# Optimization experiments

Measured on AMD Instinct MI355X. Metric: run time of the kernel, lower is better.

The kernel has to match this reference:

```python
import jax, jax.numpy as jnp
import numpy as np
from jax import lax

WS = 7            # window size
DIM = 256         # out_dim
HEADS = 8
HD = DIM // HEADS # head dim = 32
HIDDEN = 4 * DIM  # mlp hidden = 1024
IN_DIM = 512
EPS = 1e-6

def _rel_pos_index(ws):
    coords = np.stack(np.meshgrid(np.arange(ws), np.arange(ws), indexing='ij'))
    cf = coords.reshape(2, -1)
    rc = (cf[:, :, None] - cf[:, None, :]).transpose(1, 2, 0)
    rc[:, :, 0] += ws - 1
    rc[:, :, 1] += ws - 1
    rc[:, :, 0] *= 2 * ws - 1
    return rc.sum(-1)  # (N, N)

RPI = jnp.asarray(_rel_pos_index(WS))  # (49, 49) int

def _layernorm(x, g, b):
    m = jnp.mean(x, axis=-1, keepdims=True)
    v = jnp.mean(jnp.square(x - m), axis=-1, keepdims=True)
    return (x - m) * lax.rsqrt(v + EPS) * g + b

def setup_inputs() -> dict:
    key = jax.random.key(0)
    ks = jax.random.split(key, 16)
    s = 0.02
    inp = {
        'x': jax.random.normal(ks[0], (8, IN_DIM, 48, 48), jnp.float32),
        'skip_feat': jax.random.normal(ks[1], (8, DIM, 96, 96), jnp.float32),
        # ConvTranspose2d(in, out, k=2, s=2): weight (in, out, 2, 2), bias (out,)
        'up_w': jax.random.normal(ks[2], (IN_DIM, DIM, 2, 2), jnp.float32) * s,
        'up_b': jnp.zeros((DIM,), jnp.float32),
        # skip_adapter Conv2d(out, out, 1, bias=False)
        'skip_w': jax.random.normal(ks[3], (DIM, DIM, 1, 1), jnp.float32) * s,
        'gamma1': jnp.ones((DIM,), jnp.float32),
        'beta1': jnp.zeros((DIM,), jnp.float32),
        'qkv_w': jax.random.normal(ks[4], (3 * DIM, DIM), jnp.float32) * s,
        'qkv_b': jnp.zeros((3 * DIM,), jnp.float32),
        'rpb_table': jax.random.normal(ks[5], ((2 * WS - 1) ** 2, HEADS), jnp.float32) * s,
        'proj_w': jax.random.normal(ks[6], (DIM, DIM), jnp.float32) * s,
        'proj_b': jnp.zeros((DIM,), jnp.float32),
        'gamma2': jnp.ones((DIM,), jnp.float32),
        'beta2': jnp.zeros((DIM,), jnp.float32),
        'mlp_w1': jax.random.normal(ks[7], (HIDDEN, DIM), jnp.float32) * s,
        'mlp_b1': jnp.zeros((HIDDEN,), jnp.float32),
        'mlp_w2': jax.random.normal(ks[8], (DIM, HIDDEN), jnp.float32) * s,
        'mlp_b2': jnp.zeros((DIM,), jnp.float32),
    }
    return inp

def _forward(x, skip_feat, up_w, up_b, skip_w, gamma1, beta1, qkv_w, qkv_b,
             rpb_table, proj_w, proj_b, gamma2, beta2, mlp_w1, mlp_b1, mlp_w2, mlp_b2):
    B = x.shape[0]
    # ConvTranspose2d k=2 s=2 p=0 == lhs-dilated conv with spatially flipped kernel
    y = lax.conv_general_dilated(
        x, jnp.flip(up_w, (2, 3)), window_strides=(1, 1),
        padding=((1, 1), (1, 1)), lhs_dilation=(2, 2),
        dimension_numbers=('NCHW', 'IOHW', 'NCHW')) + up_b[None, :, None, None]
    shortcut = y  # (B, C, Hup, Wup)
    # skip adapter (1x1 conv, no bias); shapes match so no interpolate/adhoc conv
    y = y + jnp.einsum('oi,bihw->bohw', skip_w[:, :, 0, 0], skip_feat)
    xh = jnp.transpose(y, (0, 2, 3, 1))  # (B, H, W, C)
    H, W, C = xh.shape[1], xh.shape[2], xh.shape[3]
    xn = _layernorm(xh, gamma1, beta1)
    pad_b = (WS - H % WS) % WS
    pad_r = (WS - W % WS) % WS
    xp = jnp.pad(xn, ((0, 0), (0, pad_b), (0, pad_r), (0, 0)))
    Hp, Wp = H + pad_b, W + pad_r
    N = WS * WS
    # window partition -> (B * nWh * nWw, N, C)
    win = xp.reshape(B, Hp // WS, WS, Wp // WS, WS, C)
    win = jnp.transpose(win, (0, 1, 3, 2, 4, 5)).reshape(-1, N, C)
    B_ = win.shape[0]
    # attention
    qkv = (win @ qkv_w.T + qkv_b).reshape(B_, N, 3, HEADS, HD)
    qkv = jnp.transpose(qkv, (2, 0, 3, 1, 4))  # (3, B_, h, N, hd)
    q, k, v = qkv[0], qkv[1], qkv[2]
    attn = jnp.einsum('bhnd,bhmd->bhnm', q * (HD ** -0.5), k)
    bias = rpb_table[RPI.reshape(-1)].reshape(N, N, HEADS)
    attn = attn + jnp.transpose(bias, (2, 0, 1))[None]  # (B_, h, N, N)
    attn = jax.nn.softmax(attn, axis=-1)
    o = jnp.einsum('bhnm,bhmd->bhnd', attn, v)
    o = jnp.transpose(o, (0, 2, 1, 3)).reshape(B_, N, C)
    o = o @ proj_w.T + proj_b
    # window reverse + crop
    o = o.reshape(B, Hp // WS, Wp // WS, WS, WS, C)
    o = jnp.transpose(o, (0, 1, 3, 2, 4, 5)).reshape(B, Hp, Wp, C)[:, :H, :W]
    x2 = jnp.transpose(shortcut, (0, 2, 3, 1)) + o
    # MLP
    h = jax.nn.gelu(_layernorm(x2, gamma2, beta2) @ mlp_w1.T + mlp_b1, approximate=False)
    x3 = x2 + (h @ mlp_w2.T + mlp_b2)
    return jnp.transpose(x3, (0, 3, 1, 2))  # (B, C, Hup, Wup)

def reference(x, skip_feat, up_w, up_b, skip_w, gamma1, beta1, qkv_w, qkv_b,
              rpb_table, proj_w, proj_b, gamma2, beta2, mlp_w1, mlp_b1, mlp_w2, mlp_b2):
    return _forward(x, skip_feat, up_w, up_b, skip_w, gamma1, beta1, qkv_w, qkv_b,
                    rpb_table, proj_w, proj_b, gamma2, beta2, mlp_w1, mlp_b1, mlp_w2, mlp_b2)
```

## Files before the change

### kernel.cpp

```cpp
#include <hip/hip_runtime.h>

typedef __attribute__((ext_vector_type(8))) short short8;
typedef __attribute__((ext_vector_type(4))) float f32x4;
typedef __attribute__((ext_vector_type(4))) unsigned short u16x4;
typedef unsigned short u16;
typedef unsigned int u32;

#define DEV static __device__ __forceinline__

DEV u16 f2b(float f) {
  u32 u = __builtin_bit_cast(u32, f);
  return (u16)((u + 0x7fffu + ((u >> 16) & 1u)) >> 16);
}
DEV float b2f(u16 h) {
  u32 u = ((u32)h) << 16;
  return __builtin_bit_cast(float, u);
}
DEV short8 ld8(const u16* p) { return *reinterpret_cast<const short8*>(p); }
DEV f32x4 mfma16(short8 a, short8 b, f32x4 c) {
  return __builtin_amdgcn_mfma_f32_16x16x32_bf16(a, b, c, 0, 0, 0);
}
DEV float wredsum(float v) {
#pragma unroll
  for (int off = 1; off < 64; off <<= 1) v += __shfl_xor(v, off);
  return v;
}

#define GLL(gp, lp) __builtin_amdgcn_global_load_lds( \
    (const __attribute__((address_space(1))) void*)(gp), \
    (__attribute__((address_space(3))) void*)(lp), 16, 0, 0)

#define WQKV   0
#define WPROJ  196608
#define WM1    262144
#define WM2    524288
#define WSKIP  786432
#define WUP    851968

#define OFF_BIAS 2752512u
#define OFF_SC   2883584u
#define OFF_OVR  40632320u
#define OFF_STAT (OFF_OVR + 52000000u)
#define OFF_PST  (OFF_OVR + 52600000u)
#define OFF_SGB  (OFF_OVR + 55000000u)
#define WS_NEED  96227328u

__global__ void k_sentinel(float* out) { out[threadIdx.x] = 31337.0f; }

__global__ __launch_bounds__(256) void k_prep(
    const float* qkv_w, const float* proj_w, const float* mlp_w1,
    const float* mlp_w2, const float* skip_w, const float* up_w,
    const float* rpb, const float* g1, const float* g2, u16* W, float* bias_g) {
  int i = blockIdx.x * 256 + threadIdx.x;
  if (i < 196608) { W[WQKV + i] = f2b(qkv_w[i] * g1[i & 255]); return; }
  i -= 196608;
  if (i < 65536) { W[WPROJ + i] = f2b(proj_w[i]); return; }
  i -= 65536;
  if (i < 262144) { W[WM1 + i] = f2b(mlp_w1[i] * g2[i & 255]); return; }
  i -= 262144;
  if (i < 262144) { W[WM2 + i] = f2b(mlp_w2[i]); return; }
  i -= 262144;
  if (i < 65536) { W[WSKIP + i] = f2b(skip_w[i]); return; }
  i -= 65536;
  if (i < 524288) {
    int ci = i & 511; int rest = i >> 9; int co = rest & 255; int kk = rest >> 8;
    W[WUP + i] = f2b(up_w[ci * 1024 + co * 4 + kk]);
    return;
  }
  i -= 524288;
  if (i < 32768) {
    int h = i >> 12, r = i & 4095, ii = r >> 6, j = r & 63;
    float v;
    if (j >= 49) v = -1e30f;
    else if (ii >= 49) v = 0.f;
    else {
      int d0 = (ii / 7 - j / 7) + 6, d1 = (ii % 7 - j % 7) + 6;
      v = rpb[(d0 * 13 + d1) * 8 + h];
    }
    bias_g[i] = v;
  }
}

__global__ __launch_bounds__(256) void k_fold(
    const float* mlp_w1, const float* qkv_w, const float* g1, const float* be1,
    const float* g2, const float* be2, float* sgb) {
  int wave = threadIdx.x >> 6, lane = threadIdx.x & 63;
  int id = blockIdx.x * 4 + wave;
  const float* wsrc;
  const float* vec;
  int out;
  if (id < 1024) { wsrc = mlp_w1 + (size_t)id * 256; vec = g2; out = id; }
  else if (id < 2048) { wsrc = mlp_w1 + (size_t)(id - 1024) * 256; vec = be2; out = id; }
  else { wsrc = qkv_w + (size_t)(id - 2048) * 256; vec = be1; out = 2816 + (id - 2048); }
  float s = 0.f;
#pragma unroll
  for (int j = 0; j < 4; j++) {
    int k = j * 64 + lane;
    s += vec[k] * wsrc[k];
  }
  s = wredsum(s);
  if (lane == 0) sgb[out] = s;
}

__global__ __launch_bounds__(256) void k_tr(const float* src, u16* dst, int C, int HW) {
  __shared__ float t[32][33];
  int hw0 = blockIdx.x * 32, c0 = blockIdx.y * 32, b = blockIdx.z;
  int tx = threadIdx.x & 31, ty = threadIdx.x >> 5;
  const float* s = src + (size_t)b * C * HW;
  u16* d = dst + (size_t)b * C * HW;
#pragma unroll
  for (int i = 0; i < 4; i++)
    t[ty + i * 8][tx] = s[(size_t)(c0 + ty + i * 8) * HW + hw0 + tx];
  __syncthreads();
#pragma unroll
  for (int i = 0; i < 4; i++)
    d[(size_t)(hw0 + ty + i * 8) * C + c0 + tx] = f2b(t[tx][ty + i * 8]);
}

__global__ __launch_bounds__(256) void k_tr_skip(const float* src, u16* dst) {
  __shared__ float t[32][33];
  int w0 = blockIdx.x * 32, c0 = blockIdx.y * 32;
  int z = blockIdx.z;
  int b = z / 96, h = z - b * 96;
  int tx = threadIdx.x & 31, ty = threadIdx.x >> 5;
  const float* s = src + (size_t)b * 256 * 9216 + (size_t)h * 96;
  u16* d = dst + (((size_t)b * 96 + h) * 96) * 256;
#pragma unroll
  for (int i = 0; i < 4; i++)
    t[ty + i * 8][tx] = s[(size_t)(c0 + ty + i * 8) * 9216 + w0 + tx];
  __syncthreads();
#pragma unroll
  for (int i = 0; i < 4; i++)
    d[(size_t)(w0 + ty + i * 8) * 256 + c0 + tx] = f2b(t[tx][ty + i * 8]);
}

__global__ __launch_bounds__(256) void k1g(
    const u16* W, const u16* xt, const float* up_b, u16* sc) {
  __shared__ __align__(16) u16 Ab[2][4096];
  __shared__ __align__(16) u16 Bb[2][4096];
  int tid = threadIdx.x;
  int lane = tid & 63, wave = tid >> 6;
  int m = lane & 15, gq = lane >> 4;
  int wr = wave >> 1, wc = wave & 1;
  int bm = blockIdx.x * 128, bn = blockIdx.y * 128;
  int kk = blockIdx.z, kh = kk >> 1, kw = kk & 1;
  const u16* Ag = xt + (size_t)bm * 512;
  const u16* Bg = W + WUP + (size_t)kk * 131072 + (size_t)bn * 512;
  f32x4 acc[4][4] = {};
#pragma unroll
  for (int c = 0; c < 2; c++) {
    int flat = (wave * 2 + c) * 512 + lane * 8;
    int r = flat >> 5, cc = flat & 31;
    GLL(Ag + (size_t)r * 512 + cc, &Ab[0][(wave * 2 + c) * 512]);
    GLL(Bg + (size_t)r * 512 + cc, &Bb[0][(wave * 2 + c) * 512]);
  }
  __syncthreads();
  int cur = 0;
  for (int ki = 0; ki < 16; ki++) {
    if (ki < 15) {
      int kkk = (ki + 1) * 32;
#pragma unroll
      for (int c = 0; c < 2; c++) {
        int flat = (wave * 2 + c) * 512 + lane * 8;
        int r = flat >> 5, cc = flat & 31;
        GLL(Ag + (size_t)r * 512 + kkk + cc, &Ab[cur ^ 1][(wave * 2 + c) * 512]);
        GLL(Bg + (size_t)r * 512 + kkk + cc, &Bb[cur ^ 1][(wave * 2 + c) * 512]);
      }
    }
    short8 aF[4], bF[4];
#pragma unroll
    for (int mt = 0; mt < 4; mt++)
      aF[mt] = ld8(&Ab[cur][(wr * 64 + mt * 16 + m) * 32 + gq * 8]);
#pragma unroll
    for (int nt = 0; nt < 4; nt++)
      bF[nt] = ld8(&Bb[cur][(wc * 64 + nt * 16 + m) * 32 + gq * 8]);
#pragma unroll
    for (int mt = 0; mt < 4; mt++)
#pragma unroll
      for (int nt = 0; nt < 4; nt++)
        acc[mt][nt] = mfma16(aF[mt], bF[nt], acc[mt][nt]);
    __syncthreads();
    cur ^= 1;
  }
  float ub[4];
#pragma unroll
  for (int nt = 0; nt < 4; nt++) ub[nt] = up_b[bn + wc * 64 + nt * 16 + m];
#pragma unroll
  for (int mt = 0; mt < 4; mt++)
#pragma unroll
    for (int rr = 0; rr < 4; rr++) {
      int t = bm + wr * 64 + mt * 16 + gq * 4 + rr;
      int b = t / 2304, rem = t - b * 2304;
      int ih = rem / 48, iw = rem - ih * 48;
      int h = 2 * ih + kh, w = 2 * iw + kw;
      size_t tok = ((size_t)b * 96 + h) * 96 + w;
#pragma unroll
      for (int nt = 0; nt < 4; nt++) {
        int ch = bn + wc * 64 + nt * 16 + m;
        sc[tok * 256 + ch] = f2b(acc[mt][nt][rr] + ub[nt]);
      }
    }
}

__global__ __launch_bounds__(256) void k2y(
    const u16* W, const u16* skt, const u16* sc, u16* ybuf, float* pstat) {
  __shared__ __align__(16) u16 Ab[2][4096];
  __shared__ __align__(16) u16 Bb[2][4096];
  int tid = threadIdx.x;
  int lane = tid & 63, wave = tid >> 6;
  int m = lane & 15, gq = lane >> 4;
  int wr = wave >> 1, wc = wave & 1;
  int bm = blockIdx.x * 128, bn = blockIdx.y * 128;
  const u16* Ag = skt + (size_t)bm * 256;
  const u16* Bg = W + WSKIP + (size_t)bn * 256;
  f32x4 acc[4][4] = {};
#pragma unroll
  for (int c = 0; c < 2; c++) {
    int flat = (wave * 2 + c) * 512 + lane * 8;
    int r = flat >> 5, cc = flat & 31;
    GLL(Ag + (size_t)r * 256 + cc, &Ab[0][(wave * 2 + c) * 512]);
    GLL(Bg + (size_t)r * 256 + cc, &Bb[0][(wave * 2 + c) * 512]);
  }
  __syncthreads();
  int cur = 0;
  for (int ki = 0; ki < 8; ki++) {
    if (ki < 7) {
      int kk = (ki + 1) * 32;
#pragma unroll
      for (int c = 0; c < 2; c++) {
        int flat = (wave * 2 + c) * 512 + lane * 8;
        int r = flat >> 5, cc = flat & 31;
        GLL(Ag + (size_t)r * 256 + kk + cc, &Ab[cur ^ 1][(wave * 2 + c) * 512]);
        GLL(Bg + (size_t)r * 256 + kk + cc, &Bb[cur ^ 1][(wave * 2 + c) * 512]);
      }
    }
    short8 aF[4], bF[4];
#pragma unroll
    for (int mt = 0; mt < 4; mt++)
      aF[mt] = ld8(&Ab[cur][(wr * 64 + mt * 16 + m) * 32 + gq * 8]);
#pragma unroll
    for (int nt = 0; nt < 4; nt++)
      bF[nt] = ld8(&Bb[cur][(wc * 64 + nt * 16 + m) * 32 + gq * 8]);
#pragma unroll
    for (int mt = 0; mt < 4; mt++)
#pragma unroll
      for (int nt = 0; nt < 4; nt++)
        acc[mt][nt] = mfma16(aF[mt], bF[nt], acc[mt][nt]);
    __syncthreads();
    cur ^= 1;
  }
#pragma unroll
  for (int mt = 0; mt < 4; mt++)
#pragma unroll
    for (int rr = 0; rr < 4; rr++) {
      int tok = bm + wr * 64 + mt * 16 + gq * 4 + rr;
      float s = 0.f, s2 = 0.f;
#pragma unroll
      for (int nt = 0; nt < 4; nt++) {
        int ch = bn + wc * 64 + nt * 16 + m;
        float y = acc[mt][nt][rr] + b2f(sc[(size_t)tok * 256 + ch]);
        ybuf[(size_t)tok * 256 + ch] = f2b(y);
        s += y; s2 += y * y;
      }
#pragma unroll
      for (int off = 1; off < 16; off <<= 1) {
        s += __shfl_xor(s, off);
        s2 += __shfl_xor(s2, off);
      }
      if (m == 0) {
        int pi = (tok * 4 + blockIdx.y * 2 + wc) * 2;
        pstat[pi] = s;
        pstat[pi + 1] = s2;
      }
    }
}

__global__ __launch_bounds__(256) void k_statfin(const float* pstat, float* stat) {
  int row = blockIdx.x * 256 + threadIdx.x;
  float s = 0.f, s2 = 0.f;
#pragma unroll
  for (int j = 0; j < 4; j++) {
    s += pstat[(row * 4 + j) * 2];
    s2 += pstat[(row * 4 + j) * 2 + 1];
  }
  float mean = s * 0.00390625f;
  float var = s2 * 0.00390625f - mean * mean;
  float r = rsqrtf(var + 1e-6f);
  stat[row * 2] = r;
  stat[row * 2 + 1] = r * mean;
}

__global__ __launch_bounds__(256) void k23(
    const u16* W, const u16* ybuf, const float* stat, const float* sgb,
    const float* qkv_b, const float* bias_g, u16* obr) {
  __shared__ __align__(16) u16 yl[49 * 264];
  __shared__ __align__(16) u16 pws[4][6144];
  int tid = threadIdx.x;
  int lane = tid & 63, wave = tid >> 6;
  int m = lane & 15, gq = lane >> 4, k0 = gq * 8;
  int blk = blockIdx.x;
  int bimg = blk / 196, wl = blk - bimg * 196;
  int wrow = wl / 14, wcol = wl - wrow * 14;
  int h0 = wrow * 7, w0 = wcol * 7;
  u16* prv = pws[wave];
#pragma unroll
  for (int t = 0; t < 8; t++) {
    u16x4 z = {};
    *reinterpret_cast<u16x4*>(&prv[t * 256 + lane * 4]) = z;
  }
  for (int it = 0; it < 7; it++) {
    int flat = it * 256 + tid;
    if (flat < 1568) {
      int row = flat >> 5, cc = (flat & 31) * 8;
      int hh = h0 + row / 7, ww = w0 + row % 7;
      short8 v = {};
      if (hh < 96 && ww < 96) {
        int ras = (bimg * 96 + hh) * 96 + ww;
        short8 raw = ld8(ybuf + (size_t)ras * 256 + cc);
        float rs = stat[ras * 2], rmu = stat[ras * 2 + 1];
#pragma unroll
        for (int q2 = 0; q2 < 8; q2++) {
          float zz = b2f(((const u16*)&raw)[q2]) * rs - rmu;
          ((u16*)&v)[q2] = f2b(zz);
        }
      }
      *reinterpret_cast<short8*>(&yl[row * 264 + cc]) = v;
    }
  }
  __syncthreads();
  const float scale = 0.1767766952966369f;
#pragma unroll
  for (int hp = 0; hp < 2; hp++) {
    int h = wave * 2 + hp;
    {
      const u16* bb0 = W + WQKV + (size_t)(h * 32 + m) * 256;
      const u16* bb1 = W + WQKV + (size_t)(h * 32 + 16 + m) * 256;
      const u16* bb2 = W + WQKV + (size_t)(256 + h * 32 + m) * 256;
      const u16* bb3 = W + WQKV + (size_t)(256 + h * 32 + 16 + m) * 256;
      f32x4 acc[4][4] = {};
#pragma unroll 4
      for (int ks = 0; ks < 8; ks++) {
        short8 a[4];
#pragma unroll
        for (int mt = 0; mt < 4; mt++) {
          int row = mt * 16 + m; if (row > 48) row = 48;
          a[mt] = ld8(&yl[row * 264 + ks * 32 + k0]);
        }
        short8 b0 = ld8(bb0 + ks * 32 + k0);
        short8 b1 = ld8(bb1 + ks * 32 + k0);
        short8 b2 = ld8(bb2 + ks * 32 + k0);
        short8 b3 = ld8(bb3 + ks * 32 + k0);
#pragma unroll
        for (int mt = 0; mt < 4; mt++) {
          acc[mt][0] = mfma16(a[mt], b0, acc[mt][0]);
          acc[mt][1] = mfma16(a[mt], b1, acc[mt][1]);
          acc[mt][2] = mfma16(a[mt], b2, acc[mt][2]);
          acc[mt][3] = mfma16(a[mt], b3, acc[mt][3]);
        }
      }
#pragma unroll
      for (int nt = 0; nt < 4; nt++) {
        int hd = (nt & 1) * 16 + m;
        int c = (nt >> 1) * 256 + h * 32 + hd;
        float qb_ = qkv_b[c];
        float sb1 = sgb[2816 + c];
        int base = (nt < 2) ? 2048 : 3616;
#pragma unroll
        for (int mt = 0; mt < 4; mt++)
#pragma unroll
          for (int rr = 0; rr < 4; rr++) {
            int row = mt * 16 + gq * 4 + rr;
            if (row >= 49) continue;
            int hh = h0 + row / 7, ww = w0 + row % 7;
            float vf = (hh < 96 && ww < 96) ? 1.f : 0.f;
            prv[base + row * 32 + hd] = f2b(acc[mt][nt][rr] + vf * sb1 + qb_);
          }
      }
    }
    {
      const u16* bb0 = W + WQKV + (size_t)(512 + h * 32 + m) * 256;
      const u16* bb1 = W + WQKV + (size_t)(512 + h * 32 + 16 + m) * 256;
      f32x4 vacc[4][2] = {};
#pragma unroll 4
      for (int ks = 0; ks < 8; ks++) {
        short8 a[4];
#pragma unroll
        for (int mt = 0; mt < 4; mt++) {
          int row = mt * 16 + m; if (row > 48) row = 48;
          a[mt] = ld8(&yl[row * 264 + ks * 32 + k0]);
        }
        short8 b0 = ld8(bb0 + ks * 32 + k0);
        short8 b1 = ld8(bb1 + ks * 32 + k0);
#pragma unroll
        for (int mt = 0; mt < 4; mt++) {
          vacc[mt][0] = mfma16(a[mt], b0, vacc[mt][0]);
          vacc[mt][1] = mfma16(a[mt], b1, vacc[mt][1]);
        }
      }
      int vsw = (m & 7) * 8;
#pragma unroll
      for (int nv = 0; nv < 2; nv++) {
        int hd = nv * 16 + m;
        int c = 512 + h * 32 + hd;
        float qb_ = qkv_b[c];
        float sb1 = sgb[2816 + c];
#pragma unroll
        for (int mt = 0; mt < 4; mt++)
#pragma unroll
          for (int rr = 0; rr < 4; rr++) {
            int row = mt * 16 + gq * 4 + rr;
            if (row >= 49) continue;
            int hh = h0 + row / 7, ww = w0 + row % 7;
            float vf = (hh < 96 && ww < 96) ? 1.f : 0.f;
            prv[hd * 64 + (row ^ vsw)] = f2b(vacc[mt][nv][rr] + vf * sb1 + qb_);
          }
      }
    }
    short8 aq[4], bk[4];
#pragma unroll
    for (int mt = 0; mt < 4; mt++) { int i = mt * 16 + m; if (i > 48) i = 48; aq[mt] = ld8(&prv[2048 + i * 32 + k0]); }
#pragma unroll
    for (int nt = 0; nt < 4; nt++) { int j = nt * 16 + m; if (j > 48) j = 48; bk[nt] = ld8(&prv[3616 + j * 32 + k0]); }
    f32x4 s[4][4] = {};
#pragma unroll
    for (int mt = 0; mt < 4; mt++)
#pragma unroll
      for (int nt = 0; nt < 4; nt++)
        s[mt][nt] = mfma16(aq[mt], bk[nt], s[mt][nt]);
    const float* BI = bias_g + h * 4096;
    float rsum[4][4];
#pragma unroll
    for (int mt = 0; mt < 4; mt++)
#pragma unroll
      for (int rr = 0; rr < 4; rr++) {
        int i = mt * 16 + gq * 4 + rr;
        float sv[4];
        float mx = -1e38f;
#pragma unroll
        for (int nt = 0; nt < 4; nt++) {
          sv[nt] = s[mt][nt][rr] * scale + BI[i * 64 + nt * 16 + m];
          mx = fmaxf(mx, sv[nt]);
        }
        mx = fmaxf(mx, __shfl_xor(mx, 1));
        mx = fmaxf(mx, __shfl_xor(mx, 2));
        mx = fmaxf(mx, __shfl_xor(mx, 4));
        mx = fmaxf(mx, __shfl_xor(mx, 8));
        float sum = 0.f;
#pragma unroll
        for (int nt = 0; nt < 4; nt++) { sv[nt] = __expf(sv[nt] - mx); sum += sv[nt]; }
        sum += __shfl_xor(sum, 1);
        sum += __shfl_xor(sum, 2);
        sum += __shfl_xor(sum, 4);
        sum += __shfl_xor(sum, 8);
        rsum[mt][rr] = sum;
        int isw = (i & 7) * 8;
#pragma unroll
        for (int nt = 0; nt < 4; nt++) {
          int j = nt * 16 + m;
          prv[2048 + i * 64 + (j ^ isw)] = f2b(sv[nt]);
        }
      }
    f32x4 o[4][2] = {};
#pragma unroll
    for (int ks = 0; ks < 2; ks++) {
      short8 bv[2];
#pragma unroll
      for (int nt = 0; nt < 2; nt++) {
        int hd = nt * 16 + m;
        bv[nt] = ld8(&prv[hd * 64 + ((ks * 32 + k0) ^ ((hd & 7) * 8))]);
      }
#pragma unroll
      for (int mt = 0; mt < 4; mt++) {
        int i = mt * 16 + m;
        short8 ap = *reinterpret_cast<const short8*>(
            &prv[2048 + i * 64 + ((ks * 32 + k0) ^ ((i & 7) * 8))]);
#pragma unroll
        for (int nt = 0; nt < 2; nt++)
          o[mt][nt] = mfma16(ap, bv[nt], o[mt][nt]);
      }
    }
#pragma unroll
    for (int mt = 0; mt < 4; mt++)
#pragma unroll
      for (int rr = 0; rr < 4; rr++) {
        int i = mt * 16 + gq * 4 + rr;
        if (i >= 49) continue;
        int hh = h0 + i / 7, ww = w0 + i % 7;
        if (hh >= 96 || ww >= 96) continue;
        size_t ras = ((size_t)bimg * 96 + hh) * 96 + ww;
        float rinv = 1.f / rsum[mt][rr];
#pragma unroll
        for (int nt = 0; nt < 2; nt++) {
          int c = h * 32 + nt * 16 + m;
          obr[ras * 256 + c] = f2b(o[mt][nt][rr] * rinv);
        }
      }
  }
}

__global__ __launch_bounds__(256) void k4r(
    const u16* W, const u16* obr, const float* proj_b, u16* sc, float* pstat) {
  __shared__ __align__(16) u16 Ab[2][4096];
  __shared__ __align__(16) u16 Bb[2][4096];
  int tid = threadIdx.x;
  int lane = tid & 63, wave = tid >> 6;
  int m = lane & 15, gq = lane >> 4;
  int wr = wave >> 1, wc = wave & 1;
  int bm = blockIdx.x * 128, bn = blockIdx.y * 128;
  const u16* Ag = obr + (size_t)bm * 256;
  const u16* Bg = W + WPROJ + (size_t)bn * 256;
  f32x4 acc[4][4] = {};
#pragma unroll
  for (int c = 0; c < 2; c++) {
    int flat = (wave * 2 + c) * 512 + lane * 8;
    int r = flat >> 5, cc = flat & 31;
    GLL(Ag + (size_t)r * 256 + cc, &Ab[0][(wave * 2 + c) * 512]);
    GLL(Bg + (size_t)r * 256 + cc, &Bb[0][(wave * 2 + c) * 512]);
  }
  __syncthreads();
  int cur = 0;
  for (int ki = 0; ki < 8; ki++) {
    if (ki < 7) {
      int kk = (ki + 1) * 32;
#pragma unroll
      for (int c = 0; c < 2; c++) {
        int flat = (wave * 2 + c) * 512 + lane * 8;
        int r = flat >> 5, cc = flat & 31;
        GLL(Ag + (size_t)r * 256 + kk + cc, &Ab[cur ^ 1][(wave * 2 + c) * 512]);
        GLL(Bg + (size_t)r * 256 + kk + cc, &Bb[cur ^ 1][(wave * 2 + c) * 512]);
      }
    }
    short8 aF[4], bF[4];
#pragma unroll
    for (int mt = 0; mt < 4; mt++)
      aF[mt] = ld8(&Ab[cur][(wr * 64 + mt * 16 + m) * 32 + gq * 8]);
#pragma unroll
    for (int nt = 0; nt < 4; nt++)
      bF[nt] = ld8(&Bb[cur][(wc * 64 + nt * 16 + m) * 32 + gq * 8]);
#pragma unroll
    for (int mt = 0; mt < 4; mt++)
#pragma unroll
      for (int nt = 0; nt < 4; nt++)
        acc[mt][nt] = mfma16(aF[mt], bF[nt], acc[mt][nt]);
    __syncthreads();
    cur ^= 1;
  }
#pragma unroll
  for (int mt = 0; mt < 4; mt++)
#pragma unroll
    for (int rr = 0; rr < 4; rr++) {
      int tok = bm + wr * 64 + mt * 16 + gq * 4 + rr;
      float s = 0.f, s2 = 0.f;
#pragma unroll
      for (int nt = 0; nt < 4; nt++) {
        int ch = bn + wc * 64 + nt * 16 + m;
        float v = acc[mt][nt][rr] + proj_b[ch] + b2f(sc[(size_t)tok * 256 + ch]);
        sc[(size_t)tok * 256 + ch] = f2b(v);
        s += v; s2 += v * v;
      }
#pragma unroll
      for (int off = 1; off < 16; off <<= 1) {
        s += __shfl_xor(s, off);
        s2 += __shfl_xor(s2, off);
      }
      if (m == 0) {
        int pi = (tok * 4 + blockIdx.y * 2 + wc) * 2;
        pstat[pi] = s;
        pstat[pi + 1] = s2;
      }
    }
}

__global__ __launch_bounds__(256) void k5f(
    const u16* W, const u16* x2b, const float* stat, const float* sgb,
    const float* mb1, u16* h1q) {
  __shared__ __align__(16) u16 Ab[2][4096];
  __shared__ __align__(16) u16 Bb[2][4096];
  int tid = threadIdx.x;
  int lane = tid & 63, wave = tid >> 6;
  int m = lane & 15, gq = lane >> 4;
  int wr = wave >> 1, wc = wave & 1;
  int bm = blockIdx.x * 128, bn = blockIdx.y * 128;
  const u16* Ag = x2b + (size_t)bm * 256;
  const u16* Bg = W + WM1 + (size_t)bn * 256;
  f32x4 acc[4][4] = {};
#pragma unroll
  for (int c = 0; c < 2; c++) {
    int flat = (wave * 2 + c) * 512 + lane * 8;
    int r = flat >> 5, cc = flat & 31;
    GLL(Ag + (size_t)r * 256 + cc, &Ab[0][(wave * 2 + c) * 512]);
    GLL(Bg + (size_t)r * 256 + cc, &Bb[0][(wave * 2 + c) * 512]);
  }
  __syncthreads();
  int cur = 0;
  for (int ki = 0; ki < 8; ki++) {
    if (ki < 7) {
      int kk = (ki + 1) * 32;
#pragma unroll
      for (int c = 0; c < 2; c++) {
        int flat = (wave * 2 + c) * 512 + lane * 8;
        int r = flat >> 5, cc = flat & 31;
        GLL(Ag + (size_t)r * 256 + kk + cc, &Ab[cur ^ 1][(wave * 2 + c) * 512]);
        GLL(Bg + (size_t)r * 256 + kk + cc, &Bb[cur ^ 1][(wave * 2 + c) * 512]);
      }
    }
    short8 aF[4], bF[4];
#pragma unroll
    for (int mt = 0; mt < 4; mt++)
      aF[mt] = ld8(&Ab[cur][(wr * 64 + mt * 16 + m) * 32 + gq * 8]);
#pragma unroll
    for (int nt = 0; nt < 4; nt++)
      bF[nt] = ld8(&Bb[cur][(wc * 64 + nt * 16 + m) * 32 + gq * 8]);
#pragma unroll
    for (int mt = 0; mt < 4; mt++)
#pragma unroll
      for (int nt = 0; nt < 4; nt++)
        acc[mt][nt] = mfma16(aF[mt], bF[nt], acc[mt][nt]);
    __syncthreads();
    cur ^= 1;
  }
  float sgv[4], sbv[4], b1v[4];
#pragma unroll
  for (int nt = 0; nt < 4; nt++) {
    int ch = bn + wc * 64 + nt * 16 + m;
    sgv[nt] = sgb[ch];
    sbv[nt] = sgb[1024 + ch];
    b1v[nt] = mb1[ch];
  }
#pragma unroll
  for (int mt = 0; mt < 4; mt++)
#pragma unroll
    for (int rr = 0; rr < 4; rr++) {
      int tok = bm + wr * 64 + mt * 16 + gq * 4 + rr;
      float rs = stat[tok * 2], rmu = stat[tok * 2 + 1];
#pragma unroll
      for (int nt = 0; nt < 4; nt++) {
        float v = rs * acc[mt][nt][rr] - rmu * sgv[nt] + sbv[nt] + b1v[nt];
        v = 0.5f * v * (1.f + erff(v * 0.7071067811865475f));
        h1q[(size_t)tok * 1024 + (bn + wc * 64 + nt * 16 + m)] = f2b(v);
      }
    }
}

__global__ __launch_bounds__(256) void k6g(
    const u16* W, const u16* h1q, const float* mb2, const u16* x2b,
    float* out, int tok_base) {
  __shared__ __align__(16) u16 Ab[2][2048];
  __shared__ __align__(16) u16 Bb[2][4096];
  __shared__ float ot[128 * 66];
  int tid = threadIdx.x;
  int lane = tid & 63, wave = tid >> 6;
  int m = lane & 15, gq = lane >> 4;
  int wr = wave >> 1, wc = wave & 1;
  int bm = blockIdx.x * 64, bn = blockIdx.y * 128;
  const u16* Ag = h1q + (size_t)bm * 1024;
  const u16* Bg = W + WM2 + (size_t)bn * 1024;
  f32x4 acc[2][4] = {};
  {
    int flatA = wave * 512 + lane * 8;
    GLL(Ag + (size_t)(flatA >> 5) * 1024 + (flatA & 31), &Ab[0][wave * 512]);
#pragma unroll
    for (int c = 0; c < 2; c++) {
      int flat = (wave * 2 + c) * 512 + lane * 8;
      GLL(Bg + (size_t)(flat >> 5) * 1024 + (flat & 31), &Bb[0][(wave * 2 + c) * 512]);
    }
  }
  __syncthreads();
  int cur = 0;
  for (int ki = 0; ki < 32; ki++) {
    if (ki < 31) {
      int kk = (ki + 1) * 32;
      int flatA = wave * 512 + lane * 8;
      GLL(Ag + (size_t)(flatA >> 5) * 1024 + kk + (flatA & 31), &Ab[cur ^ 1][wave * 512]);
#pragma unroll
      for (int c = 0; c < 2; c++) {
        int flat = (wave * 2 + c) * 512 + lane * 8;
        GLL(Bg + (size_t)(flat >> 5) * 1024 + kk + (flat & 31), &Bb[cur ^ 1][(wave * 2 + c) * 512]);
      }
    }
    short8 aF[2], bF[4];
#pragma unroll
    for (int mt = 0; mt < 2; mt++)
      aF[mt] = ld8(&Ab[cur][(wr * 32 + mt * 16 + m) * 32 + gq * 8]);
#pragma unroll
    for (int nt = 0; nt < 4; nt++)
      bF[nt] = ld8(&Bb[cur][(wc * 64 + nt * 16 + m) * 32 + gq * 8]);
#pragma unroll
    for (int mt = 0; mt < 2; mt++)
#pragma unroll
      for (int nt = 0; nt < 4; nt++)
        acc[mt][nt] = mfma16(aF[mt], bF[nt], acc[mt][nt]);
    __syncthreads();
    cur ^= 1;
  }
#pragma unroll
  for (int nt = 0; nt < 4; nt++) {
    int nl = wc * 64 + nt * 16 + m;
    int ch = bn + nl;
    float bias = mb2[ch];
#pragma unroll
    for (int mt = 0; mt < 2; mt++)
#pragma unroll
      for (int rr = 0; rr < 4; rr++) {
        int tl = wr * 32 + mt * 16 + gq * 4 + rr;
        float v = acc[mt][nt][rr] + bias + b2f(x2b[(size_t)(bm + tl) * 256 + ch]);
        ot[nl * 66 + tl] = v;
      }
  }
  __syncthreads();
  int tg = tok_base + bm;
  int bimg = tg / 9216, hw0 = tg % 9216;
  for (int it = 0; it < 32; it++) {
    int flat = it * 256 + tid;
    int j = flat >> 6, t = flat & 63;
    out[((size_t)bimg * 256 + bn + j) * 9216 + hw0 + t] = ot[j * 66 + t];
  }
}

extern "C" void kernel_launch(void* const* d_in, const int* in_sizes, int n_in,
                              void* d_out, int out_size, void* d_ws, size_t ws_size,
                              hipStream_t stream) {
  const float* x      = (const float*)d_in[0];
  const float* skipf  = (const float*)d_in[1];
  const float* up_w   = (const float*)d_in[2];
  const float* up_b   = (const float*)d_in[3];
  const float* skip_w = (const float*)d_in[4];
  const float* g1     = (const float*)d_in[5];
  const float* be1    = (const float*)d_in[6];
  const float* qkv_w  = (const float*)d_in[7];
  const float* qkv_b  = (const float*)d_in[8];
  const float* rpb    = (const float*)d_in[9];
  const float* proj_w = (const float*)d_in[10];
  const float* proj_b = (const float*)d_in[11];
  const float* g2     = (const float*)d_in[12];
  const float* be2    = (const float*)d_in[13];
  const float* m_w1   = (const float*)d_in[14];
  const float* m_b1   = (const float*)d_in[15];
  const float* m_w2   = (const float*)d_in[16];
  const float* m_b2   = (const float*)d_in[17];
  if (ws_size < WS_NEED) {
    k_sentinel<<<1, 256, 0, stream>>>((float*)d_out);
    return;
  }
  char* ws = (char*)d_ws;
  u16*   W    = (u16*)ws;
  float* bias = (float*)(ws + OFF_BIAS);
  u16*   sc   = (u16*)(ws + OFF_SC);
  u16*   xt   = (u16*)(ws + OFF_OVR);
  u16*   skt  = (u16*)(ws + OFF_OVR);
  u16*   h1q  = (u16*)(ws + OFF_OVR);
  float* stat = (float*)(ws + OFF_STAT);
  float* pst  = (float*)(ws + OFF_PST);
  float* sgb  = (float*)(ws + OFF_SGB);
  u16*   ybuf = (u16*)d_out;
  u16*   obr  = (u16*)((char*)d_out + 37748736u);

  k_prep<<<5504, 256, 0, stream>>>(qkv_w, proj_w, m_w1, m_w2, skip_w, up_w, rpb,
                                   g1, g2, W, bias);
  k_fold<<<704, 256, 0, stream>>>(m_w1, qkv_w, g1, be1, g2, be2, sgb);
  k_tr<<<dim3(72, 16, 8), 256, 0, stream>>>(x, xt, 512, 2304);
  k1g<<<dim3(144, 2, 4), 256, 0, stream>>>(W, xt, up_b, sc);
  k_tr_skip<<<dim3(3, 8, 768), 256, 0, stream>>>(skipf, skt);
  k2y<<<dim3(576, 2), 256, 0, stream>>>(W, skt, sc, ybuf, pst);
  k_statfin<<<288, 256, 0, stream>>>(pst, stat);
  k23<<<1568, 256, 0, stream>>>(W, ybuf, stat, sgb, qkv_b, bias, obr);
  k4r<<<dim3(576, 2), 256, 0, stream>>>(W, obr, proj_b, sc, pst);
  k_statfin<<<288, 256, 0, stream>>>(pst, stat);
  for (int q = 0; q < 4; q++) {
    const u16* x2b = sc + (size_t)q * 18432 * 256;
    k5f<<<dim3(144, 8), 256, 0, stream>>>(W, x2b, stat + (size_t)q * 36864,
                                          sgb, m_b1, h1q);
    k6g<<<dim3(288, 2), 256, 0, stream>>>(W, h1q, m_b2, x2b, (float*)d_out, q * 18432);
  }
}
```

Baseline: 646.4 us.

## Fuse MLP fc1+GELU and fc2 into one kernel keeping hidden in LDS

```diff
diff --git a/kernel.cpp b/kernel.cpp
--- a/kernel.cpp
+++ b/kernel.cpp
@@ -571,149 +571,118 @@
     }
 }
 
-__global__ __launch_bounds__(256) void k5f(
-    const u16* W, const u16* x2b, const float* stat, const float* sgb,
-    const float* mb1, u16* h1q) {
-  __shared__ __align__(16) u16 Ab[2][4096];
-  __shared__ __align__(16) u16 Bb[2][4096];
+__global__ __launch_bounds__(256) void k56(
+    const u16* W, const u16* x2, const float* stat, const float* sgb,
+    const float* mb1, const float* mb2, float* out) {
+  __shared__ __align__(16) u16 XA[64 * 264];
+  __shared__ __align__(16) u16 HC[64 * 136];
   int tid = threadIdx.x;
   int lane = tid & 63, wave = tid >> 6;
-  int m = lane & 15, gq = lane >> 4;
-  int wr = wave >> 1, wc = wave & 1;
-  int bm = blockIdx.x * 128, bn = blockIdx.y * 128;
-  const u16* Ag = x2b + (size_t)bm * 256;
-  const u16* Bg = W + WM1 + (size_t)bn * 256;
-  f32x4 acc[4][4] = {};
-#pragma unroll
-  for (int c = 0; c < 2; c++) {
-    int flat = (wave * 2 + c) * 512 + lane * 8;
-    int r = flat >> 5, cc = flat & 31;
-    GLL(Ag + (size_t)r * 256 + cc, &Ab[0][(wave * 2 + c) * 512]);
-    GLL(Bg + (size_t)r * 256 + cc, &Bb[0][(wave * 2 + c) * 512]);
+  int m = lane & 15, gq = lane >> 4, k0 = gq * 8;
+  int tok0 = blockIdx.x * 64;
+#pragma unroll
+  for (int it = 0; it < 8; it++) {
+    int flat = it * 2048 + tid * 8;
+    int row = flat >> 8, col = flat & 255;
+    *reinterpret_cast<short8*>(&XA[row * 264 + col]) =
+        ld8(x2 + (size_t)(tok0 + row) * 256 + col);
   }
   __syncthreads();
-  int cur = 0;
-  for (int ki = 0; ki < 8; ki++) {
-    if (ki < 7) {
-      int kk = (ki + 1) * 32;
-#pragma unroll
-      for (int c = 0; c < 2; c++) {
-        int flat = (wave * 2 + c) * 512 + lane * 8;
-        int r = flat >> 5, cc = flat & 31;
-        GLL(Ag + (size_t)r * 256 + kk + cc, &Ab[cur ^ 1][(wave * 2 + c) * 512]);
-        GLL(Bg + (size_t)r * 256 + kk + cc, &Bb[cur ^ 1][(wave * 2 + c) * 512]);
-      }
-    }
-    short8 aF[4], bF[4];
-#pragma unroll
-    for (int mt = 0; mt < 4; mt++)
-      aF[mt] = ld8(&Ab[cur][(wr * 64 + mt * 16 + m) * 32 + gq * 8]);
-#pragma unroll
-    for (int nt = 0; nt < 4; nt++)
-      bF[nt] = ld8(&Bb[cur][(wc * 64 + nt * 16 + m) * 32 + gq * 8]);
-#pragma unroll
-    for (int mt = 0; mt < 4; mt++)
-#pragma unroll
-      for (int nt = 0; nt < 4; nt++)
-        acc[mt][nt] = mfma16(aF[mt], bF[nt], acc[mt][nt]);
+  f32x4 acc2[4][4] = {};
+  for (int c = 0; c < 8; c++) {
+    const u16* B1a = W + WM1 + (size_t)(c * 128 + wave * 32 + m) * 256;
+    const u16* B1b = W + WM1 + (size_t)(c * 128 + wave * 32 + 16 + m) * 256;
+    f32x4 acc1[4][2] = {};
+#pragma unroll 4
+    for (int ks = 0; ks < 8; ks++) {
+      short8 a[4];
+#pragma unroll
+      for (int mt = 0; mt < 4; mt++)
+        a[mt] = ld8(&XA[(mt * 16 + m) * 264 + ks * 32 + k0]);
+      short8 b0 = ld8(B1a + ks * 32 + k0);
+      short8 b1 = ld8(B1b + ks * 32 + k0);
+#pragma unroll
+      for (int mt = 0; mt < 4; mt++) {
+        acc1[mt][0] = mfma16(a[mt], b0, acc1[mt][0]);
+        acc1[mt][1] = mfma16(a[mt], b1, acc1[mt][1]);
+      }
+    }
+#pragma unroll
+    for (int nt = 0; nt < 2; nt++) {
+      int col = wave * 32 + nt * 16 + m;
+      int ch = c * 128 + col;
+      float sg = sgb[ch], sb = sgb[1024 + ch], b1v = mb1[ch];
+#pragma unroll
+      for (int mt = 0; mt < 4; mt++)
+#pragma unroll
+        for (int rr = 0; rr < 4; rr++) {
+          int tl = mt * 16 + gq * 4 + rr;
+          int tok = tok0 + tl;
+          float rs = stat[tok * 2], rmu = stat[tok * 2 + 1];
+          float v = rs * acc1[mt][nt][rr] - rmu * sg + sb + b1v;
+          v = 0.5f * v * (1.f + erff(v * 0.7071067811865475f));
+          HC[tl * 136 + col] = f2b(v);
+        }
+    }
     __syncthreads();
-    cur ^= 1;
-  }
-  float sgv[4], sbv[4], b1v[4];
+#pragma unroll
+    for (int ks = 0; ks < 4; ks++) {
+      short8 a2[4];
+#pragma unroll
+      for (int mt = 0; mt < 4; mt++)
+        a2[mt] = ld8(&HC[(mt * 16 + m) * 136 + ks * 32 + k0]);
+      short8 bF[4];
+#pragma unroll
+      for (int nt = 0; nt < 4; nt++) {
+        int ch = wave * 64 + nt * 16 + m;
+        bF[nt] = ld8(W + WM2 + (size_t)ch * 1024 + c * 128 + ks * 32 + k0);
+      }
+#pragma unroll
+      for (int mt = 0; mt < 4; mt++)
+#pragma unroll
+        for (int nt = 0; nt < 4; nt++)
+          acc2[mt][nt] = mfma16(a2[mt], bF[nt], acc2[mt][nt]);
+    }
+    __syncthreads();
+  }
 #pragma unroll
   for (int nt = 0; nt < 4; nt++) {
-    int ch = bn + wc * 64 + nt * 16 + m;
-    sgv[nt] = sgb[ch];
-    sbv[nt] = sgb[1024 + ch];
-    b1v[nt] = mb1[ch];
-  }
-#pragma unroll
-  for (int mt = 0; mt < 4; mt++)
-#pragma unroll
-    for (int rr = 0; rr < 4; rr++) {
-      int tok = bm + wr * 64 + mt * 16 + gq * 4 + rr;
-      float rs = stat[tok * 2], rmu = stat[tok * 2 + 1];
+    int ch = wave * 64 + nt * 16 + m;
+    float bias = mb2[ch];
+#pragma unroll
+    for (int mt = 0; mt < 4; mt++)
+#pragma unroll
+      for (int rr = 0; rr < 4; rr++) {
+        int tl = mt * 16 + gq * 4 + rr;
+        acc2[mt][nt][rr] += bias + b2f(XA[tl * 264 + ch]);
+      }
+  }
+  __syncthreads();
+  float* ot = (float*)XA;
+  int tg = tok0;
+  int bimg = tg / 9216, hw0 = tg % 9216;
+#pragma unroll
+  for (int half = 0; half < 2; half++) {
+    if ((wave >> 1) == half) {
 #pragma unroll
       for (int nt = 0; nt < 4; nt++) {
-        float v = rs * acc[mt][nt][rr] - rmu * sgv[nt] + sbv[nt] + b1v[nt];
-        v = 0.5f * v * (1.f + erff(v * 0.7071067811865475f));
-        h1q[(size_t)tok * 1024 + (bn + wc * 64 + nt * 16 + m)] = f2b(v);
-      }
-    }
-}
-
-__global__ __launch_bounds__(256) void k6g(
-    const u16* W, const u16* h1q, const float* mb2, const u16* x2b,
-    float* out, int tok_base) {
-  __shared__ __align__(16) u16 Ab[2][2048];
-  __shared__ __align__(16) u16 Bb[2][4096];
-  __shared__ float ot[128 * 66];
-  int tid = threadIdx.x;
-  int lane = tid & 63, wave = tid >> 6;
-  int m = lane & 15, gq = lane >> 4;
-  int wr = wave >> 1, wc = wave & 1;
-  int bm = blockIdx.x * 64, bn = blockIdx.y * 128;
-  const u16* Ag = h1q + (size_t)bm * 1024;
-  const u16* Bg = W + WM2 + (size_t)bn * 1024;
-  f32x4 acc[2][4] = {};
-  {
-    int flatA = wave * 512 + lane * 8;
-    GLL(Ag + (size_t)(flatA >> 5) * 1024 + (flatA & 31), &Ab[0][wave * 512]);
-#pragma unroll
-    for (int c = 0; c < 2; c++) {
-      int flat = (wave * 2 + c) * 512 + lane * 8;
-      GLL(Bg + (size_t)(flat >> 5) * 1024 + (flat & 31), &Bb[0][(wave * 2 + c) * 512]);
-    }
-  }
-  __syncthreads();
-  int cur = 0;
-  for (int ki = 0; ki < 32; ki++) {
-    if (ki < 31) {
-      int kk = (ki + 1) * 32;
-      int flatA = wave * 512 + lane * 8;
-      GLL(Ag + (size_t)(flatA >> 5) * 1024 + kk + (flatA & 31), &Ab[cur ^ 1][wave * 512]);
-#pragma unroll
-      for (int c = 0; c < 2; c++) {
-        int flat = (wave * 2 + c) * 512 + lane * 8;
-        GLL(Bg + (size_t)(flat >> 5) * 1024 + kk + (flat & 31), &Bb[cur ^ 1][(wave * 2 + c) * 512]);
-      }
-    }
-    short8 aF[2], bF[4];
-#pragma unroll
-    for (int mt = 0; mt < 2; mt++)
-      aF[mt] = ld8(&Ab[cur][(wr * 32 + mt * 16 + m) * 32 + gq * 8]);
-#pragma unroll
-    for (int nt = 0; nt < 4; nt++)
-      bF[nt] = ld8(&Bb[cur][(wc * 64 + nt * 16 + m) * 32 + gq * 8]);
-#pragma unroll
-    for (int mt = 0; mt < 2; mt++)
-#pragma unroll
-      for (int nt = 0; nt < 4; nt++)
-        acc[mt][nt] = mfma16(aF[mt], bF[nt], acc[mt][nt]);
+        int jj = (wave & 1) * 64 + nt * 16 + m;
+#pragma unroll
+        for (int mt = 0; mt < 4; mt++)
+#pragma unroll
+          for (int rr = 0; rr < 4; rr++) {
+            int tl = mt * 16 + gq * 4 + rr;
+            ot[jj * 66 + tl] = acc2[mt][nt][rr];
+          }
+      }
+    }
     __syncthreads();
-    cur ^= 1;
-  }
-#pragma unroll
-  for (int nt = 0; nt < 4; nt++) {
-    int nl = wc * 64 + nt * 16 + m;
-    int ch = bn + nl;
-    float bias = mb2[ch];
-#pragma unroll
-    for (int mt = 0; mt < 2; mt++)
-#pragma unroll
-      for (int rr = 0; rr < 4; rr++) {
-        int tl = wr * 32 + mt * 16 + gq * 4 + rr;
-        float v = acc[mt][nt][rr] + bias + b2f(x2b[(size_t)(bm + tl) * 256 + ch]);
-        ot[nl * 66 + tl] = v;
-      }
-  }
-  __syncthreads();
-  int tg = tok_base + bm;
-  int bimg = tg / 9216, hw0 = tg % 9216;
-  for (int it = 0; it < 32; it++) {
-    int flat = it * 256 + tid;
-    int j = flat >> 6, t = flat & 63;
-    out[((size_t)bimg * 256 + bn + j) * 9216 + hw0 + t] = ot[j * 66 + t];
+    for (int it = 0; it < 32; it++) {
+      int flat = it * 256 + tid;
+      int j = flat >> 6, t = flat & 63;
+      out[((size_t)bimg * 256 + half * 128 + j) * 9216 + hw0 + t] = ot[j * 66 + t];
+    }
+    __syncthreads();
   }
 }
 
@@ -748,7 +717,6 @@
   u16*   sc   = (u16*)(ws + OFF_SC);
   u16*   xt   = (u16*)(ws + OFF_OVR);
   u16*   skt  = (u16*)(ws + OFF_OVR);
-  u16*   h1q  = (u16*)(ws + OFF_OVR);
   float* stat = (float*)(ws + OFF_STAT);
   float* pst  = (float*)(ws + OFF_PST);
   float* sgb  = (float*)(ws + OFF_SGB);
@@ -766,10 +734,5 @@
   k23<<<1568, 256, 0, stream>>>(W, ybuf, stat, sgb, qkv_b, bias, obr);
   k4r<<<dim3(576, 2), 256, 0, stream>>>(W, obr, proj_b, sc, pst);
   k_statfin<<<288, 256, 0, stream>>>(pst, stat);
-  for (int q = 0; q < 4; q++) {
-    const u16* x2b = sc + (size_t)q * 18432 * 256;
-    k5f<<<dim3(144, 8), 256, 0, stream>>>(W, x2b, stat + (size_t)q * 36864,
-                                          sgb, m_b1, h1q);
-    k6g<<<dim3(288, 2), 256, 0, stream>>>(W, h1q, m_b2, x2b, (float*)d_out, q * 18432);
-  }
-}
+  k56<<<1152, 256, 0, stream>>>(W, sc, stat, sgb, m_b1, m_b2, (float*)d_out);
+}
```

Result: faster. 602.1 us (-6.9%).
